# Kernel tuning notes

Measured on AMD Instinct MI355X. Metric: run time of the kernel, lower is better.

## Reference

```python
import jax, jax.numpy as jnp
import numpy as np

N_NODES = 100000
N_EDGES = 3200000
IN_CH = 256


def setup_inputs() -> dict:
    key = jax.random.key(0)
    ks = jax.random.split(key, 8)
    x = jax.random.normal(ks[0], (N_NODES, IN_CH), dtype=jnp.float32)
    edge_index = jax.random.randint(ks[1], (2, N_EDGES), 0, N_NODES, dtype=jnp.int64)
    alpha = jnp.ones((), dtype=jnp.float32)
    beta = jnp.ones((), dtype=jnp.float32)
    s = 1.0 / np.sqrt(IN_CH)
    W_mlp = jax.random.normal(ks[2], (1, IN_CH), dtype=jnp.float32) * s
    W_lin = jax.random.normal(ks[3], (1, IN_CH), dtype=jnp.float32) * s
    W_gcn = jax.random.normal(ks[4], (1, IN_CH), dtype=jnp.float32) * s
    W_att = jax.random.normal(ks[5], (3, 3), dtype=jnp.float32) * (1.0 / np.sqrt(3))
    b_att = jax.random.normal(ks[6], (3,), dtype=jnp.float32) * 0.1
    return {"x": x, "edge_index": edge_index, "alpha": alpha, "beta": beta,
            "W_mlp": W_mlp, "W_lin": W_lin, "W_gcn": W_gcn,
            "W_att": W_att, "b_att": b_att}


def _gcn_conv(x, edge_index, W_gcn, num_nodes):
    # PyG GCNConv: add self-loops, symmetric normalization, no bias.
    loop = jnp.arange(num_nodes, dtype=edge_index.dtype)
    row = jnp.concatenate([edge_index[0], loop])  # source
    col = jnp.concatenate([edge_index[1], loop])  # target
    deg = jax.ops.segment_sum(jnp.ones_like(col, dtype=x.dtype), col,
                              num_segments=num_nodes)
    dinv = jnp.where(deg > 0, jax.lax.rsqrt(deg), 0.0)
    norm = dinv[row] * dinv[col]                  # [E+N]
    xw = x @ W_gcn.T                               # [N, 1]
    msg = norm[:, None] * xw[row]                  # [E+N, 1]
    return jax.ops.segment_sum(msg, col, num_segments=num_nodes)  # [N, 1]


def reference(x, edge_index, alpha, beta, W_mlp, W_lin, W_gcn, W_att, b_att):
    num_nodes = x.shape[0]
    # score1: in-degree based
    deg = jax.ops.segment_sum(jnp.ones((edge_index.shape[1],), dtype=x.dtype),
                              edge_index[1], num_segments=num_nodes)
    score1 = jax.nn.sigmoid(alpha * jnp.sqrt(deg) + beta)           # [N]
    # score2: tiny MLP
    score2 = jax.nn.sigmoid((x @ W_mlp.T)[:, 0])                    # [N]
    # score3: GCNConv + linear
    gcn_out = _gcn_conv(x, edge_index, W_gcn, num_nodes)            # [N,1]
    score3 = jax.nn.sigmoid((gcn_out + x @ W_lin.T)[:, 0])          # [N]
    scores = jnp.stack([score1, score2, score3], axis=1)            # [N,3]
    weight = jax.nn.softmax(scores @ W_att.T + b_att, axis=1)       # [N,3]
    fitness = jnp.sum(weight * scores, axis=1)                      # [N]
    return fitness
```

## Files before the change

### kernel.cpp

```cpp
#include <hip/hip_runtime.h>
#include <math.h>

#define N_CH   256
#define BSHIFT 7
#define NPB    128
#define NBMAX  1024
#define EPB_H  16384
#define EPB_S  4096

__device__ __forceinline__ float sigmoidf_(float v) {
    return 1.0f / (1.0f + expf(-v));
}

__global__ __launch_bounds__(256) void dots_hist_kernel(
    const float* __restrict__ x,
    const float* __restrict__ Wmlp, const float* __restrict__ Wlin,
    const float* __restrict__ Wgcn, const int* __restrict__ dst,
    float* __restrict__ s2dot, float* __restrict__ s3lin, float* __restrict__ xw,
    int* __restrict__ totals,
    int n_nodes, int n_edges, int nb, int histBlocks)
{
    __shared__ int h[NBMAX];
    if ((int)blockIdx.x < histBlocks) {
        for (int i = threadIdx.x; i < nb; i += 256) h[i] = 0;
        __syncthreads();
        int start = blockIdx.x * EPB_H;
        #pragma unroll 4
        for (int k = 0; k < EPB_H / 1024; ++k) {
            int e = start + (k * 256 + (int)threadIdx.x) * 4;
            if (e + 3 < n_edges) {
                int4 d4 = *(const int4*)(dst + e);
                atomicAdd(&h[d4.x >> BSHIFT], 1);
                atomicAdd(&h[d4.y >> BSHIFT], 1);
                atomicAdd(&h[d4.z >> BSHIFT], 1);
                atomicAdd(&h[d4.w >> BSHIFT], 1);
            } else {
                for (int ee = e; ee < n_edges; ++ee)
                    atomicAdd(&h[dst[ee] >> BSHIFT], 1);
            }
        }
        __syncthreads();
        for (int b = threadIdx.x; b < nb; b += 256)
            if (h[b]) atomicAdd(&totals[b], h[b]);
        return;
    }

    int wid  = ((int)blockIdx.x - histBlocks) * 4 + ((int)threadIdx.x >> 6);
    int lane = threadIdx.x & 63;
    if (wid >= n_nodes) return;

    const float4* xr = (const float4*)(x + (size_t)wid * N_CH);
    float4 v  = xr[lane];
    float4 wm = ((const float4*)Wmlp)[lane];
    float4 wl = ((const float4*)Wlin)[lane];
    float4 wg = ((const float4*)Wgcn)[lane];

    float d0 = v.x*wm.x + v.y*wm.y + v.z*wm.z + v.w*wm.w;
    float d1 = v.x*wl.x + v.y*wl.y + v.z*wl.z + v.w*wl.w;
    float d2 = v.x*wg.x + v.y*wg.y + v.z*wg.z + v.w*wg.w;

    #pragma unroll
    for (int off = 32; off; off >>= 1) {
        d0 += __shfl_down(d0, off, 64);
        d1 += __shfl_down(d1, off, 64);
        d2 += __shfl_down(d2, off, 64);
    }
    if (lane == 0) { s2dot[wid] = d0; s3lin[wid] = d1; xw[wid] = d2; }
}

__global__ __launch_bounds__(1024) void scan_kernel(
    const int* __restrict__ totals, int* __restrict__ bs,
    int* __restrict__ cursor, int nb)
{
    __shared__ int s[1024];
    int t = threadIdx.x;
    int v = (t < nb) ? totals[t] : 0;
    s[t] = v;
    __syncthreads();
    for (int off = 1; off < 1024; off <<= 1) {
        int a = s[t];
        int b = (t >= off) ? s[t - off] : 0;
        __syncthreads();
        s[t] = a + b;
        __syncthreads();
    }
    if (t < nb) { int e = s[t] - v; bs[t] = e; cursor[t] = e; }
    if (t == 1023) bs[nb] = s[1023];
}

__global__ __launch_bounds__(256) void scatter_kernel(
    const int* __restrict__ src, const int* __restrict__ dst,
    int* __restrict__ cursor, int* __restrict__ bpack,
    int n_edges, int nb)
{
    __shared__ int h[NBMAX];
    __shared__ int base[NBMAX];
    for (int i = threadIdx.x; i < nb; i += 256) h[i] = 0;
    __syncthreads();

    int start = blockIdx.x * EPB_S;
    #pragma unroll 4
    for (int k = 0; k < EPB_S / 1024; ++k) {
        int e = start + (k * 256 + (int)threadIdx.x) * 4;
        if (e + 3 < n_edges) {
            int4 d4 = *(const int4*)(dst + e);
            atomicAdd(&h[d4.x >> BSHIFT], 1);
            atomicAdd(&h[d4.y >> BSHIFT], 1);
            atomicAdd(&h[d4.z >> BSHIFT], 1);
            atomicAdd(&h[d4.w >> BSHIFT], 1);
        } else {
            for (int ee = e; ee < n_edges; ++ee)
                atomicAdd(&h[dst[ee] >> BSHIFT], 1);
        }
    }
    __syncthreads();
    for (int b = threadIdx.x; b < nb; b += 256) {
        int c = h[b];
        base[b] = c ? atomicAdd(&cursor[b], c) : 0;
        h[b] = 0;
    }
    __syncthreads();
    #pragma unroll 4
    for (int k = 0; k < EPB_S / 1024; ++k) {
        int e = start + (k * 256 + (int)threadIdx.x) * 4;
        if (e + 3 < n_edges) {
            int4 s4 = *(const int4*)(src + e);
            int4 d4 = *(const int4*)(dst + e);
            int ss[4] = {s4.x, s4.y, s4.z, s4.w};
            int dd[4] = {d4.x, d4.y, d4.z, d4.w};
            #pragma unroll
            for (int j = 0; j < 4; ++j) {
                int b = dd[j] >> BSHIFT;
                int r = atomicAdd(&h[b], 1);
                bpack[base[b] + r] = ss[j] | ((dd[j] & (NPB - 1)) << 17);
            }
        } else {
            for (int ee = e; ee < n_edges; ++ee) {
                int d = dst[ee];
                int b = d >> BSHIFT;
                int r = atomicAdd(&h[b], 1);
                bpack[base[b] + r] = src[ee] | ((d & (NPB - 1)) << 17);
            }
        }
    }
}

__global__ __launch_bounds__(256) void degdinv_kernel(
    const int* __restrict__ bpack, const int* __restrict__ bs,
    const float* __restrict__ xw,
    float* __restrict__ degf, float* __restrict__ dinv, float* __restrict__ sxw,
    int n_nodes)
{
    __shared__ int cnt[NPB];
    int b = blockIdx.x, t = threadIdx.x;
    if (t < NPB) cnt[t] = 0;
    __syncthreads();
    int e0 = bs[b], e1 = bs[b + 1];
    for (int e = e0 + t; e < e1; e += 256)
        atomicAdd(&cnt[bpack[e] >> 17], 1);
    __syncthreads();
    int node0 = b << BSHIFT;
    if (t < NPB && node0 + t < n_nodes) {
        int i = node0 + t;
        float d = (float)cnt[t];
        degf[i] = d;
        float di = rsqrtf(d + 1.0f);
        dinv[i] = di;
        sxw[i]  = di * xw[i];
    }
}

__global__ __launch_bounds__(256) void gather_final_kernel(
    const int* __restrict__ bpack, const int* __restrict__ bs,
    const float* __restrict__ sxw, const float* __restrict__ dinv,
    const float* __restrict__ degf, const float* __restrict__ s2dot,
    const float* __restrict__ s3lin, const float* __restrict__ xw,
    const float* __restrict__ alpha, const float* __restrict__ beta,
    const float* __restrict__ Watt, const float* __restrict__ batt,
    float* __restrict__ out, int n_nodes)
{
    __shared__ float acc[NPB];
    int b = blockIdx.x, t = threadIdx.x;
    if (t < NPB) acc[t] = 0.0f;
    __syncthreads();
    int e0 = bs[b], e1 = bs[b + 1];
    for (int e = e0 + t; e < e1; e += 256) {
        int p = bpack[e];
        atomicAdd(&acc[p >> 17], sxw[p & 0x1FFFF]);
    }
    __syncthreads();
    int node0 = b << BSHIFT;
    if (t < NPB && node0 + t < n_nodes) {
        int i = node0 + t;
        float dn = dinv[i];
        float g  = acc[t] * dn + dn * dn * xw[i];
        float s1 = sigmoidf_(alpha[0] * sqrtf(degf[i]) + beta[0]);
        float s2 = sigmoidf_(s2dot[i]);
        float s3 = sigmoidf_(g + s3lin[i]);

        float z0 = Watt[0]*s1 + Watt[1]*s2 + Watt[2]*s3 + batt[0];
        float z1 = Watt[3]*s1 + Watt[4]*s2 + Watt[5]*s3 + batt[1];
        float z2 = Watt[6]*s1 + Watt[7]*s2 + Watt[8]*s3 + batt[2];

        float m  = fmaxf(z0, fmaxf(z1, z2));
        float e0f = expf(z0 - m), e1f = expf(z1 - m), e2f = expf(z2 - m);
        float inv = 1.0f / (e0f + e1f + e2f);
        out[i] = (e0f * s1 + e1f * s2 + e2f * s3) * inv;
    }
}

extern "C" void kernel_launch(void* const* d_in, const int* in_sizes, int n_in,
                              void* d_out, int out_size, void* d_ws, size_t ws_size,
                              hipStream_t stream) {
    const float* x     = (const float*)d_in[0];
    const int*   ei    = (const int*)d_in[1];
    const float* alpha = (const float*)d_in[2];
    const float* beta  = (const float*)d_in[3];
    const float* Wmlp  = (const float*)d_in[4];
    const float* Wlin  = (const float*)d_in[5];
    const float* Wgcn  = (const float*)d_in[6];
    const float* Watt  = (const float*)d_in[7];
    const float* batt  = (const float*)d_in[8];
    float* out = (float*)d_out;

    int n_nodes = in_sizes[0] / N_CH;
    int n_edges = in_sizes[1] / 2;
    const int* src = ei;
    const int* dst = ei + n_edges;

    int nb = (n_nodes + NPB - 1) >> BSHIFT;
    int histBlocks    = (n_edges + EPB_H - 1) / EPB_H;
    int scatterBlocks = (n_edges + EPB_S - 1) / EPB_S;

    size_t off = 0;
    int*   bpack  = (int*)d_ws;          off += (((size_t)n_edges + 1023) & ~(size_t)1023);
    int*   totals = (int*)d_ws + off;    off += 1024;
    int*   bs     = (int*)d_ws + off;    off += 1024;
    int*   cursor = (int*)d_ws + off;    off += 1024;
    float* s2dot  = (float*)d_ws + off;  off += (((size_t)n_nodes + 1023) & ~(size_t)1023);
    float* s3lin  = (float*)d_ws + off;  off += (((size_t)n_nodes + 1023) & ~(size_t)1023);
    float* xw     = (float*)d_ws + off;  off += (((size_t)n_nodes + 1023) & ~(size_t)1023);
    float* degf   = (float*)d_ws + off;  off += (((size_t)n_nodes + 1023) & ~(size_t)1023);
    float* dinv   = (float*)d_ws + off;  off += (((size_t)n_nodes + 1023) & ~(size_t)1023);
    float* sxw    = (float*)d_ws + off;  off += (((size_t)n_nodes + 1023) & ~(size_t)1023);

    hipMemsetAsync(totals, 0, 1024 * sizeof(int), stream);

    int dotsBlocks = (n_nodes + 3) / 4;
    dots_hist_kernel<<<histBlocks + dotsBlocks, 256, 0, stream>>>(
        x, Wmlp, Wlin, Wgcn, dst, s2dot, s3lin, xw, totals,
        n_nodes, n_edges, nb, histBlocks);

    scan_kernel<<<1, 1024, 0, stream>>>(totals, bs, cursor, nb);

    scatter_kernel<<<scatterBlocks, 256, 0, stream>>>(
        src, dst, cursor, bpack, n_edges, nb);

    degdinv_kernel<<<nb, 256, 0, stream>>>(bpack, bs, xw, degf, dinv, sxw, n_nodes);

    gather_final_kernel<<<nb, 256, 0, stream>>>(
        bpack, bs, sxw, dinv, degf, s2dot, s3lin, xw,
        alpha, beta, Watt, batt, out, n_nodes);
}
```

Measured before the change: 272.7 us.

## Split edge bucketing scatter into two-level radix passes for write locality

Replaces the single scatter into 782 fine buckets with two passes: first scatter edges into 49 coarse superbuckets of 2048 nodes, then re-scatter each superbucket's contiguous range into the fine 128-node buckets. The scan kernel now also derives superbucket offsets and cursors from the fine bucket prefix sums. The aim is to cut the scattered, poorly coalesced global writes of the single pass. In exchange it adds a full extra read and write pass over the edges, plus a binary search per element to find its superbucket.

Result: faster. 259.2 us (-5.0%).

```diff
diff --git a/kernel.cpp b/kernel.cpp
--- a/kernel.cpp
+++ b/kernel.cpp
@@ -1,12 +1,16 @@
 #include <hip/hip_runtime.h>
 #include <math.h>
 
-#define N_CH   256
-#define BSHIFT 7
-#define NPB    128
-#define NBMAX  1024
-#define EPB_H  16384
-#define EPB_S  4096
+#define N_CH    256
+#define BSHIFT  7
+#define NPB     128
+#define NBMAX   1024
+#define SBSHIFT 11
+#define SBN     2048
+#define NSMAX   64
+#define EPB_H   16384
+#define EPB1    4096
+#define EPB2    4096
 
 __device__ __forceinline__ float sigmoidf_(float v) {
     return 1.0f / (1.0f + expf(-v));
@@ -35,7 +39,7 @@
                 atomicAdd(&h[d4.z >> BSHIFT], 1);
                 atomicAdd(&h[d4.w >> BSHIFT], 1);
             } else {
-                for (int ee = e; ee < n_edges; ++ee)
+                for (int ee = e; ee < n_edges && ee >= 0; ++ee)
                     atomicAdd(&h[dst[ee] >> BSHIFT], 1);
             }
         }
@@ -70,7 +74,8 @@
 
 __global__ __launch_bounds__(1024) void scan_kernel(
     const int* __restrict__ totals, int* __restrict__ bs,
-    int* __restrict__ cursor, int nb)
+    int* __restrict__ cursor2, int* __restrict__ sbs, int* __restrict__ cursor1,
+    int nb, int ns, int n_edges)
 {
     __shared__ int s[1024];
     int t = threadIdx.x;
@@ -84,44 +89,53 @@
         s[t] = a + b;
         __syncthreads();
     }
-    if (t < nb) { int e = s[t] - v; bs[t] = e; cursor[t] = e; }
+    if (t < nb) { int e = s[t] - v; bs[t] = e; cursor2[t] = e; }
     if (t == 1023) bs[nb] = s[1023];
-}
-
-__global__ __launch_bounds__(256) void scatter_kernel(
+    __syncthreads();
+    if (t < ns) {
+        int f = t << 4;
+        if (f > nb) f = nb;
+        int v2 = bs[f];
+        sbs[t] = v2;
+        cursor1[t] = v2;
+    }
+    if (t == 0) sbs[ns] = n_edges;
+}
+
+__global__ __launch_bounds__(256) void scatter1_kernel(
     const int* __restrict__ src, const int* __restrict__ dst,
-    int* __restrict__ cursor, int* __restrict__ bpack,
-    int n_edges, int nb)
-{
-    __shared__ int h[NBMAX];
-    __shared__ int base[NBMAX];
-    for (int i = threadIdx.x; i < nb; i += 256) h[i] = 0;
-    __syncthreads();
-
-    int start = blockIdx.x * EPB_S;
+    int* __restrict__ cursor1, int* __restrict__ cpack,
+    int n_edges, int ns)
+{
+    __shared__ int h[NSMAX];
+    __shared__ int base[NSMAX];
+    if (threadIdx.x < NSMAX) h[threadIdx.x] = 0;
+    __syncthreads();
+
+    int start = blockIdx.x * EPB1;
     #pragma unroll 4
-    for (int k = 0; k < EPB_S / 1024; ++k) {
+    for (int k = 0; k < EPB1 / 1024; ++k) {
         int e = start + (k * 256 + (int)threadIdx.x) * 4;
         if (e + 3 < n_edges) {
             int4 d4 = *(const int4*)(dst + e);
-            atomicAdd(&h[d4.x >> BSHIFT], 1);
-            atomicAdd(&h[d4.y >> BSHIFT], 1);
-            atomicAdd(&h[d4.z >> BSHIFT], 1);
-            atomicAdd(&h[d4.w >> BSHIFT], 1);
+            atomicAdd(&h[d4.x >> SBSHIFT], 1);
+            atomicAdd(&h[d4.y >> SBSHIFT], 1);
+            atomicAdd(&h[d4.z >> SBSHIFT], 1);
+            atomicAdd(&h[d4.w >> SBSHIFT], 1);
         } else {
-            for (int ee = e; ee < n_edges; ++ee)
-                atomicAdd(&h[dst[ee] >> BSHIFT], 1);
-        }
-    }
-    __syncthreads();
-    for (int b = threadIdx.x; b < nb; b += 256) {
-        int c = h[b];
-        base[b] = c ? atomicAdd(&cursor[b], c) : 0;
-        h[b] = 0;
+            for (int ee = e; ee < n_edges && ee >= 0; ++ee)
+                atomicAdd(&h[dst[ee] >> SBSHIFT], 1);
+        }
+    }
+    __syncthreads();
+    if (threadIdx.x < (unsigned)ns) {
+        int c = h[threadIdx.x];
+        base[threadIdx.x] = c ? atomicAdd(&cursor1[threadIdx.x], c) : 0;
+        h[threadIdx.x] = 0;
     }
     __syncthreads();
     #pragma unroll 4
-    for (int k = 0; k < EPB_S / 1024; ++k) {
+    for (int k = 0; k < EPB1 / 1024; ++k) {
         int e = start + (k * 256 + (int)threadIdx.x) * 4;
         if (e + 3 < n_edges) {
             int4 s4 = *(const int4*)(src + e);
@@ -130,16 +144,90 @@
             int dd[4] = {d4.x, d4.y, d4.z, d4.w};
             #pragma unroll
             for (int j = 0; j < 4; ++j) {
-                int b = dd[j] >> BSHIFT;
-                int r = atomicAdd(&h[b], 1);
-                bpack[base[b] + r] = ss[j] | ((dd[j] & (NPB - 1)) << 17);
+                int sb = dd[j] >> SBSHIFT;
+                int r = atomicAdd(&h[sb], 1);
+                cpack[base[sb] + r] = ss[j] | ((dd[j] & (SBN - 1)) << 17);
             }
         } else {
-            for (int ee = e; ee < n_edges; ++ee) {
+            for (int ee = e; ee < n_edges && ee >= 0; ++ee) {
                 int d = dst[ee];
-                int b = d >> BSHIFT;
-                int r = atomicAdd(&h[b], 1);
-                bpack[base[b] + r] = src[ee] | ((d & (NPB - 1)) << 17);
+                int sb = d >> SBSHIFT;
+                int r = atomicAdd(&h[sb], 1);
+                cpack[base[sb] + r] = src[ee] | ((d & (SBN - 1)) << 17);
+            }
+        }
+    }
+}
+
+__global__ __launch_bounds__(256) void scatter2_kernel(
+    const int* __restrict__ cpack, const int* __restrict__ sbs,
+    int* __restrict__ cursor2, int* __restrict__ bpack,
+    int n_edges, int nb, int ns)
+{
+    __shared__ int sbs_l[NSMAX + 1];
+    __shared__ int h[NBMAX];
+    __shared__ int base[NBMAX];
+    if (threadIdx.x <= (unsigned)ns) sbs_l[threadIdx.x] = sbs[threadIdx.x];
+    for (int i = threadIdx.x; i < nb; i += 256) h[i] = 0;
+    __syncthreads();
+
+    int start = blockIdx.x * EPB2;
+
+    #pragma unroll 4
+    for (int k = 0; k < EPB2 / 1024; ++k) {
+        int p0 = start + (k * 256 + (int)threadIdx.x) * 4;
+        int lo = 0, hi = ns;
+        while (hi - lo > 1) { int mid = (lo + hi) >> 1; if (sbs_l[mid] <= p0) lo = mid; else hi = mid; }
+        int sb = lo;
+        if (p0 + 3 < n_edges) {
+            int4 w4 = *(const int4*)(cpack + p0);
+            int ww[4] = {w4.x, w4.y, w4.z, w4.w};
+            #pragma unroll
+            for (int j = 0; j < 4; ++j) {
+                while (p0 + j >= sbs_l[sb + 1]) ++sb;
+                int l11 = ww[j] >> 17;
+                atomicAdd(&h[(sb << 4) + (l11 >> BSHIFT)], 1);
+            }
+        } else {
+            for (int p = p0; p < n_edges && p >= 0; ++p) {
+                while (p >= sbs_l[sb + 1]) ++sb;
+                int l11 = cpack[p] >> 17;
+                atomicAdd(&h[(sb << 4) + (l11 >> BSHIFT)], 1);
+            }
+        }
+    }
+    __syncthreads();
+    for (int b = threadIdx.x; b < nb; b += 256) {
+        int c = h[b];
+        base[b] = c ? atomicAdd(&cursor2[b], c) : 0;
+        h[b] = 0;
+    }
+    __syncthreads();
+    #pragma unroll 4
+    for (int k = 0; k < EPB2 / 1024; ++k) {
+        int p0 = start + (k * 256 + (int)threadIdx.x) * 4;
+        int lo = 0, hi = ns;
+        while (hi - lo > 1) { int mid = (lo + hi) >> 1; if (sbs_l[mid] <= p0) lo = mid; else hi = mid; }
+        int sb = lo;
+        if (p0 + 3 < n_edges) {
+            int4 w4 = *(const int4*)(cpack + p0);
+            int ww[4] = {w4.x, w4.y, w4.z, w4.w};
+            #pragma unroll
+            for (int j = 0; j < 4; ++j) {
+                while (p0 + j >= sbs_l[sb + 1]) ++sb;
+                int l11 = ww[j] >> 17;
+                int fb  = (sb << 4) + (l11 >> BSHIFT);
+                int r = atomicAdd(&h[fb], 1);
+                bpack[base[fb] + r] = (ww[j] & 0x1FFFF) | ((l11 & (NPB - 1)) << 17);
+            }
+        } else {
+            for (int p = p0; p < n_edges && p >= 0; ++p) {
+                while (p >= sbs_l[sb + 1]) ++sb;
+                int w = cpack[p];
+                int l11 = w >> 17;
+                int fb  = (sb << 4) + (l11 >> BSHIFT);
+                int r = atomicAdd(&h[fb], 1);
+                bpack[base[fb] + r] = (w & 0x1FFFF) | ((l11 & (NPB - 1)) << 17);
             }
         }
     }
@@ -229,20 +317,25 @@
     const int* dst = ei + n_edges;
 
     int nb = (n_nodes + NPB - 1) >> BSHIFT;
-    int histBlocks    = (n_edges + EPB_H - 1) / EPB_H;
-    int scatterBlocks = (n_edges + EPB_S - 1) / EPB_S;
+    int ns = (n_nodes + SBN - 1) >> SBSHIFT;
+    int histBlocks = (n_edges + EPB_H - 1) / EPB_H;
+    int blocks1    = (n_edges + EPB1 - 1) / EPB1;
+    int blocks2    = (n_edges + EPB2 - 1) / EPB2;
 
     size_t off = 0;
-    int*   bpack  = (int*)d_ws;          off += (((size_t)n_edges + 1023) & ~(size_t)1023);
-    int*   totals = (int*)d_ws + off;    off += 1024;
-    int*   bs     = (int*)d_ws + off;    off += 1024;
-    int*   cursor = (int*)d_ws + off;    off += 1024;
-    float* s2dot  = (float*)d_ws + off;  off += (((size_t)n_nodes + 1023) & ~(size_t)1023);
-    float* s3lin  = (float*)d_ws + off;  off += (((size_t)n_nodes + 1023) & ~(size_t)1023);
-    float* xw     = (float*)d_ws + off;  off += (((size_t)n_nodes + 1023) & ~(size_t)1023);
-    float* degf   = (float*)d_ws + off;  off += (((size_t)n_nodes + 1023) & ~(size_t)1023);
-    float* dinv   = (float*)d_ws + off;  off += (((size_t)n_nodes + 1023) & ~(size_t)1023);
-    float* sxw    = (float*)d_ws + off;  off += (((size_t)n_nodes + 1023) & ~(size_t)1023);
+    int*   cpack   = (int*)d_ws;          off += (((size_t)n_edges + 1023) & ~(size_t)1023);
+    int*   bpack   = (int*)d_ws + off;    off += (((size_t)n_edges + 1023) & ~(size_t)1023);
+    int*   totals  = (int*)d_ws + off;    off += 1024;
+    int*   bs      = (int*)d_ws + off;    off += 1024;
+    int*   cursor2 = (int*)d_ws + off;    off += 1024;
+    int*   sbs     = (int*)d_ws + off;    off += 128;
+    int*   cursor1 = (int*)d_ws + off;    off += 128;
+    float* s2dot   = (float*)d_ws + off;  off += (((size_t)n_nodes + 1023) & ~(size_t)1023);
+    float* s3lin   = (float*)d_ws + off;  off += (((size_t)n_nodes + 1023) & ~(size_t)1023);
+    float* xw      = (float*)d_ws + off;  off += (((size_t)n_nodes + 1023) & ~(size_t)1023);
+    float* degf    = (float*)d_ws + off;  off += (((size_t)n_nodes + 1023) & ~(size_t)1023);
+    float* dinv    = (float*)d_ws + off;  off += (((size_t)n_nodes + 1023) & ~(size_t)1023);
+    float* sxw     = (float*)d_ws + off;  off += (((size_t)n_nodes + 1023) & ~(size_t)1023);
 
     hipMemsetAsync(totals, 0, 1024 * sizeof(int), stream);
 
@@ -251,10 +344,14 @@
         x, Wmlp, Wlin, Wgcn, dst, s2dot, s3lin, xw, totals,
         n_nodes, n_edges, nb, histBlocks);
 
-    scan_kernel<<<1, 1024, 0, stream>>>(totals, bs, cursor, nb);
-
-    scatter_kernel<<<scatterBlocks, 256, 0, stream>>>(
-        src, dst, cursor, bpack, n_edges, nb);
+    scan_kernel<<<1, 1024, 0, stream>>>(totals, bs, cursor2, sbs, cursor1,
+                                        nb, ns, n_edges);
+
+    scatter1_kernel<<<blocks1, 256, 0, stream>>>(src, dst, cursor1, cpack,
+                                                 n_edges, ns);
+
+    scatter2_kernel<<<blocks2, 256, 0, stream>>>(cpack, sbs, cursor2, bpack,
+                                                 n_edges, nb, ns);
 
     degdinv_kernel<<<nb, 256, 0, stream>>>(bpack, bs, xw, degf, dinv, sxw, n_nodes);
 
```
